# Performance work log

Measured on AMD Instinct MI355X. Metric: run time of the kernel, lower is better.

The kernel has to match this reference:

```python
import jax, jax.numpy as jnp
import numpy as np

D_MODEL = 1024
N_LAYERS = 4
D_INNER = 2 * D_MODEL          # expand=2
D_STATE = 16
D_CONV = 4
DT_RANK = D_MODEL // 16        # ceil(1024/16)=64
B, T = 2, 1024


def setup_inputs() -> dict:
    key = jax.random.key(0)
    ks = jax.random.split(key, 8)
    s = 0.02
    return {
        "x": jax.random.normal(ks[0], (B, T, D_MODEL), jnp.float32),
        "in_proj_w": jax.random.normal(ks[1], (N_LAYERS, 2 * D_INNER, D_MODEL), jnp.float32) * s,
        "conv_w": jax.random.normal(ks[2], (N_LAYERS, D_INNER, D_CONV), jnp.float32) * s,
        "conv_b": jnp.zeros((N_LAYERS, D_INNER), jnp.float32),
        "x_proj_w": jax.random.normal(ks[3], (N_LAYERS, DT_RANK + 2 * D_STATE, D_INNER), jnp.float32) * s,
        "dt_proj_w": jax.random.normal(ks[4], (N_LAYERS, D_INNER, DT_RANK), jnp.float32) * s,
        "dt_proj_b": jax.random.normal(ks[5], (N_LAYERS, D_INNER), jnp.float32) * 0.1,
        "A_log": jnp.tile(jnp.log(jnp.arange(1.0, D_STATE + 1.0, dtype=jnp.float32)), (N_LAYERS, D_INNER, 1)),
        "Dd": jnp.ones((N_LAYERS, D_INNER), jnp.float32),
        "out_proj_w": jax.random.normal(ks[6], (N_LAYERS, D_MODEL, D_INNER), jnp.float32) * s,
        "norm_w": jnp.ones((D_MODEL,), jnp.float32),
        "norm_b": jnp.zeros((D_MODEL,), jnp.float32),
    }


def _silu(v):
    return v * jax.nn.sigmoid(v)


def _mamba_block(x, in_w, cw, cb, xp_w, dtp_w, dtp_b, A_log, Dv, out_w):
    # x: [B,T,d_model]
    xz = jnp.einsum('btd,ed->bte', x, in_w)            # [B,T,2*d_inner]
    u, z = jnp.split(xz, 2, axis=-1)                   # each [B,T,d_inner]
    # causal depthwise conv over time
    uc = jax.lax.conv_general_dilated(
        u.transpose(0, 2, 1),                          # [B,d_inner,T]
        cw[:, None, :],                                # [d_inner,1,K]
        window_strides=(1,), padding=[(D_CONV - 1, 0)],
        feature_group_count=D_INNER,
        dimension_numbers=('NCH', 'OIH', 'NCH'))
    uc = _silu(uc.transpose(0, 2, 1) + cb)             # [B,T,d_inner]
    x_dbl = jnp.einsum('btd,ed->bte', uc, xp_w)        # [B,T,dt_rank+2*d_state]
    dt_r = x_dbl[..., :DT_RANK]
    Bm = x_dbl[..., DT_RANK:DT_RANK + D_STATE]         # [B,T,d_state]
    Cm = x_dbl[..., DT_RANK + D_STATE:]                # [B,T,d_state]
    dt = jax.nn.softplus(jnp.einsum('btr,dr->btd', dt_r, dtp_w) + dtp_b)  # [B,T,d_inner]
    A = -jnp.exp(A_log)                                # [d_inner,d_state]

    def step(h, inp):
        u_t, dt_t, B_t, C_t = inp                      # [B,dI],[B,dI],[B,dS],[B,dS]
        h = jnp.exp(dt_t[..., None] * A) * h + (dt_t * u_t)[..., None] * B_t[:, None, :]
        return h, jnp.einsum('bds,bs->bd', h, C_t)

    h0 = jnp.zeros((x.shape[0], D_INNER, D_STATE), x.dtype)
    xs = (uc.transpose(1, 0, 2), dt.transpose(1, 0, 2), Bm.transpose(1, 0, 2), Cm.transpose(1, 0, 2))
    _, ys = jax.lax.scan(step, h0, xs)                 # ys: [T,B,d_inner]
    y = ys.transpose(1, 0, 2) + uc * Dv                # skip term D*u
    y = y * _silu(z)                                   # gated
    return jnp.einsum('btd,ed->bte', y, out_w)         # [B,T,d_model]


def reference(x, in_proj_w, conv_w, conv_b, x_proj_w, dt_proj_w, dt_proj_b, A_log, Dd, out_proj_w, norm_w, norm_b):
    for i in range(in_proj_w.shape[0]):
        residual = x
        x = _mamba_block(x, in_proj_w[i], conv_w[i], conv_b[i], x_proj_w[i],
                         dt_proj_w[i], dt_proj_b[i], A_log[i], Dd[i], out_proj_w[i])
        x = x + residual
    mu = jnp.mean(x, -1, keepdims=True)
    var = jnp.var(x, -1, keepdims=True)
    return (x - mu) / jnp.sqrt(var + 1e-5) * norm_w + norm_b
```

## Files before the change

### kernel.cpp

```cpp
#include <hip/hip_runtime.h>
#include <hip/hip_bf16.h>

#define N_LAYERS 4
#define D_MODEL  1024
#define D_INNER  2048
#define D_STATE  16
#define D_CONV   4
#define DT_RANK  64
#define BB       2
#define TT       1024
#define BT       (BB*TT)

#define NCHUNK 32
#define SCTC   (TT/NCHUNK)
#define TB     8

#define XP_KS  8

typedef unsigned short ushort_t;
typedef __attribute__((ext_vector_type(8))) short short8;
typedef __attribute__((ext_vector_type(8))) unsigned short ushort8_t;
typedef __attribute__((ext_vector_type(4))) float f32x4;

__device__ __forceinline__ float sigmoidf_(float x){ return 1.f/(1.f+__expf(-x)); }
__device__ __forceinline__ float siluf_(float x){ return x*sigmoidf_(x); }
__device__ __forceinline__ float softplusf_(float x){ return fmaxf(x,0.f) + log1pf(__expf(-fabsf(x))); }
__device__ __forceinline__ ushort_t f2b(float f){
    unsigned int x = __builtin_bit_cast(unsigned int, f);
    unsigned int r = (x + 0x7fffu + ((x>>16)&1u)) >> 16;
    return (ushort_t)r;
}
__device__ __forceinline__ float b2f(ushort_t u){
    unsigned int x = ((unsigned int)u) << 16;
    return __builtin_bit_cast(float, x);
}

#define GLOAD(g, l) __builtin_amdgcn_global_load_lds( \
    (const __attribute__((address_space(1))) void*)(g), \
    (__attribute__((address_space(3))) void*)(l), 16, 0, 0)

__global__ __launch_bounds__(256) void f2ball_k(
    const float* __restrict__ x, const float* __restrict__ in_w,
    const float* __restrict__ out_w, const float* __restrict__ dtp_w,
    ushort_t* __restrict__ xinb, ushort_t* __restrict__ winb,
    ushort_t* __restrict__ woutb, ushort_t* __restrict__ dtpb)
{
    const int n0 = (BT*1024)/8;
    const int n1 = (N_LAYERS*4096*1024)/8;
    const int n2 = (N_LAYERS*1024*2048)/8;
    int i = blockIdx.x*256 + threadIdx.x;
    const float4* src; ushort8_t* dst; int j;
    if (i < n0){ src=(const float4*)x; dst=(ushort8_t*)xinb; j=i; }
    else if (i < n0+n1){ src=(const float4*)in_w; dst=(ushort8_t*)winb; j=i-n0; }
    else if (i < n0+n1+n2){ src=(const float4*)out_w; dst=(ushort8_t*)woutb; j=i-n0-n1; }
    else { src=(const float4*)dtp_w; dst=(ushort8_t*)dtpb; j=i-n0-n1-n2; }
    float4 v0 = src[2*j], v1 = src[2*j+1];
    ushort8_t o;
    o[0]=f2b(v0.x); o[1]=f2b(v0.y); o[2]=f2b(v0.z); o[3]=f2b(v0.w);
    o[4]=f2b(v1.x); o[5]=f2b(v1.y); o[6]=f2b(v1.z); o[7]=f2b(v1.w);
    dst[j] = o;
}

__global__ __launch_bounds__(512) void gemm_ip(
    const ushort_t* __restrict__ A, const ushort_t* __restrict__ W,
    int M, int N, int K, ushort_t* __restrict__ outb,
    int RM, int RN, int XN)
{
    __shared__ ushort_t As[4][128*32];
    __shared__ ushort_t Ws[4][128*32];
    const int tid  = threadIdx.x;
    const int lane = tid & 63;
    const int wv   = tid >> 6;
    const int wm0  = (wv>>2)*64, wn0 = (wv&3)*32;

    const int bid = blockIdx.x;
    const int xcd = bid & 7, bi = bid >> 3;
    const int xm = xcd / XN, xn = xcd - xm*XN;
    const int m0 = (xm*RM + bi/RN)*128;
    const int n0 = (xn*RN + bi - (bi/RN)*RN)*128;

    const int r0 = tid>>2, ch = tid&3;

    f32x4 acc[4][2];
    #pragma unroll
    for (int i=0;i<4;++i)
        #pragma unroll
        for (int j=0;j<2;++j) acc[i][j] = (f32x4){0.f,0.f,0.f,0.f};

    const int row_a = lane & 15, kc = (lane>>4)*8;
    const ushort_t* gA = A + (size_t)(m0+r0)*K + ch*8;
    const ushort_t* gW = W + (size_t)(n0+r0)*K + ch*8;

#define STAGE(KT, BUF) { \
    GLOAD(gA + (KT)*32, (char*)&As[BUF][0] + tid*16); \
    GLOAD(gW + (KT)*32, (char*)&Ws[BUF][0] + tid*16); }

#define COMPUTE(BUF) { \
    short8 af[4], bf[2]; \
    _Pragma("unroll") \
    for (int i=0;i<4;++i) af[i] = *(const short8*)&As[BUF][(wm0 + i*16 + row_a)*32 + kc]; \
    _Pragma("unroll") \
    for (int j=0;j<2;++j) bf[j] = *(const short8*)&Ws[BUF][(wn0 + j*16 + row_a)*32 + kc]; \
    __builtin_amdgcn_s_setprio(1); \
    _Pragma("unroll") \
    for (int i=0;i<4;++i) \
        _Pragma("unroll") \
        for (int j=0;j<2;++j) \
            acc[i][j] = __builtin_amdgcn_mfma_f32_16x16x32_bf16(af[i], bf[j], acc[i][j], 0,0,0); \
    __builtin_amdgcn_s_setprio(0); }

    const int nt = K >> 5;
    STAGE(0, 0); STAGE(1, 1); STAGE(2, 2);
    for (int t = 0; t < nt-3; ++t){
        asm volatile("s_waitcnt vmcnt(4)" ::: "memory");
        asm volatile("s_barrier" ::: "memory");
        STAGE(t+3, (t+3)&3);
        COMPUTE(t&3);
    }
    asm volatile("s_waitcnt vmcnt(4)" ::: "memory");
    asm volatile("s_barrier" ::: "memory");
    COMPUTE((nt-3)&3);
    asm volatile("s_waitcnt vmcnt(2)" ::: "memory");
    asm volatile("s_barrier" ::: "memory");
    COMPUTE((nt-2)&3);
    asm volatile("s_waitcnt vmcnt(0)" ::: "memory");
    asm volatile("s_barrier" ::: "memory");
    COMPUTE((nt-1)&3);
#undef STAGE
#undef COMPUTE

    const int crow = (lane>>4)*4, ccol = lane & 15;
    #pragma unroll
    for (int i=0;i<4;++i){
        #pragma unroll
        for (int j=0;j<2;++j){
            #pragma unroll
            for (int r=0;r<4;++r){
                int m = m0 + wm0 + i*16 + crow + r;
                int n = n0 + wn0 + j*16 + ccol;
                outb[(size_t)m*N + n] = f2b(acc[i][j][r]);
            }
        }
    }
}

__global__ __launch_bounds__(256) void gemm_op(
    const ushort_t* __restrict__ A, const ushort_t* __restrict__ W,
    float* __restrict__ C, int M, int N, int K,
    const float* __restrict__ res, ushort_t* __restrict__ outb,
    int RM, int RN, int XN)
{
    __shared__ ushort_t As[6][64*32];
    __shared__ ushort_t Ws[6][64*32];
    const int tid  = threadIdx.x;
    const int lane = tid & 63;
    const int wv   = tid >> 6;
    const int wm0  = (wv>>1)*32, wn0 = (wv&1)*32;

    const int bid = blockIdx.x;
    const int xcd = bid & 7, bi = bid >> 3;
    const int xm = xcd / XN, xn = xcd - xm*XN;
    const int m0 = (xm*RM + bi/RN)*64;
    const int n0 = (xn*RN + bi - (bi/RN)*RN)*64;

    const int r0 = tid>>2, ch = tid&3;

    f32x4 acc[2][2];
    #pragma unroll
    for (int i=0;i<2;++i)
        #pragma unroll
        for (int j=0;j<2;++j) acc[i][j] = (f32x4){0.f,0.f,0.f,0.f};

    const int row_a = lane & 15, kc = (lane>>4)*8;
    const ushort_t* gA = A + (size_t)(m0+r0)*K + ch*8;
    const ushort_t* gW = W + (size_t)(n0+r0)*K + ch*8;

#define STAGE(KT, BUF) { \
    GLOAD(gA + (KT)*32, (char*)&As[BUF][0] + tid*16); \
    GLOAD(gW + (KT)*32, (char*)&Ws[BUF][0] + tid*16); }

#define COMPUTE(BUF) { \
    short8 af[2], bf[2]; \
    _Pragma("unroll") \
    for (int i=0;i<2;++i) af[i] = *(const short8*)&As[BUF][(wm0 + i*16 + row_a)*32 + kc]; \
    _Pragma("unroll") \
    for (int j=0;j<2;++j) bf[j] = *(const short8*)&Ws[BUF][(wn0 + j*16 + row_a)*32 + kc]; \
    _Pragma("unroll") \
    for (int i=0;i<2;++i) \
        _Pragma("unroll") \
        for (int j=0;j<2;++j) \
            acc[i][j] = __builtin_amdgcn_mfma_f32_16x16x32_bf16(af[i], bf[j], acc[i][j], 0,0,0); }

    const int np = K >> 6;
    STAGE(0, 0); STAGE(1, 1);
    STAGE(2, 2); STAGE(3, 3);
    for (int p = 0; p < np-2; ++p){
        const int bA = (p%3)*2, bS = ((p+2)%3)*2;
        asm volatile("s_waitcnt vmcnt(4)" ::: "memory");
        asm volatile("s_barrier" ::: "memory");
        STAGE(2*p+4, bS); STAGE(2*p+5, bS+1);
        __builtin_amdgcn_s_setprio(1);
        COMPUTE(bA); COMPUTE(bA+1);
        __builtin_amdgcn_s_setprio(0);
    }
    {
        const int bA = ((np-2)%3)*2;
        asm volatile("s_waitcnt vmcnt(4)" ::: "memory");
        asm volatile("s_barrier" ::: "memory");
        COMPUTE(bA); COMPUTE(bA+1);
    }
    {
        const int bA = ((np-1)%3)*2;
        asm volatile("s_waitcnt vmcnt(0)" ::: "memory");
        asm volatile("s_barrier" ::: "memory");
        COMPUTE(bA); COMPUTE(bA+1);
    }
#undef STAGE
#undef COMPUTE

    const int crow = (lane>>4)*4, ccol = lane & 15;
    #pragma unroll
    for (int i=0;i<2;++i){
        #pragma unroll
        for (int j=0;j<2;++j){
            #pragma unroll
            for (int r=0;r<4;++r){
                int m = m0 + wm0 + i*16 + crow + r;
                int n = n0 + wn0 + j*16 + ccol;
                float v = acc[i][j][r] + res[(size_t)m*N + n];
                C[(size_t)m*N + n] = v;
                outb[(size_t)m*N + n] = f2b(v);
            }
        }
    }
}

__global__ __launch_bounds__(256) void dt_mfma(
    const ushort_t* __restrict__ A, const ushort_t* __restrict__ W,
    const float* __restrict__ bias, ushort_t* __restrict__ dtb, int N)
{
    __shared__ ushort_t As[2][64*32];
    __shared__ ushort_t Ws[2][64*32];
    const int tid = threadIdx.x, lane = tid&63, wv = tid>>6;
    const int wm0 = (wv>>1)*32, wn0 = (wv&1)*32;
    const int m0 = blockIdx.y*64, n0 = blockIdx.x*64;
    const int r0 = tid>>2, ch = tid&3;
    const ushort_t* gA = A + (size_t)(m0+r0)*64 + ch*8;
    const ushort_t* gW = W + (size_t)(n0+r0)*64 + ch*8;
    GLOAD(gA,      (char*)&As[0][0] + tid*16);
    GLOAD(gW,      (char*)&Ws[0][0] + tid*16);
    GLOAD(gA + 32, (char*)&As[1][0] + tid*16);
    GLOAD(gW + 32, (char*)&Ws[1][0] + tid*16);

    f32x4 acc[2][2];
    #pragma unroll
    for (int i=0;i<2;++i)
        #pragma unroll
        for (int j=0;j<2;++j) acc[i][j] = (f32x4){0.f,0.f,0.f,0.f};

    asm volatile("s_waitcnt vmcnt(0)" ::: "memory");
    asm volatile("s_barrier" ::: "memory");
    const int row_a = lane&15, kc = (lane>>4)*8;
    #pragma unroll
    for (int buf=0; buf<2; ++buf){
        short8 af[2], bf[2];
        #pragma unroll
        for (int i=0;i<2;++i) af[i] = *(const short8*)&As[buf][(wm0 + i*16 + row_a)*32 + kc];
        #pragma unroll
        for (int j=0;j<2;++j) bf[j] = *(const short8*)&Ws[buf][(wn0 + j*16 + row_a)*32 + kc];
        #pragma unroll
        for (int i=0;i<2;++i)
            #pragma unroll
            for (int j=0;j<2;++j)
                acc[i][j] = __builtin_amdgcn_mfma_f32_16x16x32_bf16(af[i], bf[j], acc[i][j], 0,0,0);
    }

    const int crow = (lane>>4)*4, ccol = lane & 15;
    #pragma unroll
    for (int i=0;i<2;++i){
        #pragma unroll
        for (int j=0;j<2;++j){
            #pragma unroll
            for (int r=0;r<4;++r){
                int m = m0 + wm0 + i*16 + crow + r;
                int n = n0 + wn0 + j*16 + ccol;
                float v = softplusf_(acc[i][j][r] + bias[n]);
                dtb[(size_t)m*N + n] = f2b(v);
            }
        }
    }
}

__global__ __launch_bounds__(256) void conv_silu_k(
    const ushort_t* __restrict__ xzb, const float* __restrict__ cw,
    const float* __restrict__ cb, ushort_t* __restrict__ ucb)
{
    int idx = blockIdx.x*256 + threadIdx.x;
    int d8 = (idx & 255) << 3;
    int bt = idx >> 8;
    int t  = bt & (TT-1);
    ushort8_t z8 = (ushort8_t)0;
    ushort8_t r0 = (t>=3) ? *(const ushort8_t*)(xzb + (size_t)(bt-3)*4096 + d8) : z8;
    ushort8_t r1 = (t>=2) ? *(const ushort8_t*)(xzb + (size_t)(bt-2)*4096 + d8) : z8;
    ushort8_t r2 = (t>=1) ? *(const ushort8_t*)(xzb + (size_t)(bt-1)*4096 + d8) : z8;
    ushort8_t r3 = *(const ushort8_t*)(xzb + (size_t)bt*4096 + d8);
    ushort8_t o;
    #pragma unroll
    for (int j=0;j<8;++j){
        float4 w4 = *(const float4*)(cw + (size_t)(d8+j)*4);
        float a = cb[d8+j];
        a = fmaf(b2f(r0[j]), w4.x, a);
        a = fmaf(b2f(r1[j]), w4.y, a);
        a = fmaf(b2f(r2[j]), w4.z, a);
        a = fmaf(b2f(r3[j]), w4.w, a);
        o[j] = f2b(siluf_(a));
    }
    *(ushort8_t*)(ucb + (size_t)bt*D_INNER + d8) = o;
}

__global__ __launch_bounds__(256) void gemm_tn_sk(
    const ushort_t* __restrict__ A, int lda,
    const float* __restrict__ W, int ldw,
    float* __restrict__ P, int M, int N, int K)
{
    __shared__ float As[16][68];
    __shared__ float Ws[16][68];
    const int tid = threadIdx.x;
    const int tx = tid & 15, ty = tid >> 4;
    const int m0 = blockIdx.y * 64, n0 = blockIdx.x * 64;
    const int kbase = blockIdx.z * (K/XP_KS);
    const int lr = tid >> 2;
    const int lk = (tid & 3) << 2;
    float acc[4][4] = {{0.f}};

    for (int kk = 0; kk < K/XP_KS; kk += 16) {
        int k0 = kbase + kk;
        ushort4 av4 = *(const ushort4*)(A + (size_t)(m0+lr)*lda + k0 + lk);
        float4 wv = make_float4(0.f,0.f,0.f,0.f);
        if (n0 + lr < N) wv = *(const float4*)(W + (size_t)(n0+lr)*ldw + k0 + lk);
        __syncthreads();
        As[lk+0][lr]=b2f(av4.x); As[lk+1][lr]=b2f(av4.y);
        As[lk+2][lr]=b2f(av4.z); As[lk+3][lr]=b2f(av4.w);
        Ws[lk+0][lr]=wv.x; Ws[lk+1][lr]=wv.y; Ws[lk+2][lr]=wv.z; Ws[lk+3][lr]=wv.w;
        __syncthreads();
        #pragma unroll
        for (int k = 0; k < 16; ++k) {
            float4 a = *(const float4*)&As[k][ty<<2];
            float4 b = *(const float4*)&Ws[k][tx<<2];
            float a4[4] = {a.x,a.y,a.z,a.w};
            float b4[4] = {b.x,b.y,b.z,b.w};
            #pragma unroll
            for (int i=0;i<4;++i)
                #pragma unroll
                for (int j=0;j<4;++j)
                    acc[i][j] = fmaf(a4[i], b4[j], acc[i][j]);
        }
    }

    float* Pz = P + (size_t)blockIdx.z * M * 96;
    #pragma unroll
    for (int i=0;i<4;++i){
        int m = m0 + (ty<<2) + i;
        #pragma unroll
        for (int j=0;j<4;++j){
            int n = n0 + (tx<<2) + j;
            if (n < N) Pz[(size_t)m*96 + n] = acc[i][j];
        }
    }
}

__global__ __launch_bounds__(256) void sk_reduce(
    const float* __restrict__ P, float* __restrict__ outp,
    ushort_t* __restrict__ dtrb, int MN)
{
    int g = blockIdx.x*256 + threadIdx.x;
    float s = 0.f;
    #pragma unroll
    for (int ks=0; ks<XP_KS; ++ks) s += P[(size_t)ks*MN + g];
    outp[g] = s;
    int m = g / 96, c = g - m*96;
    if (c < 64) dtrb[(size_t)m*64 + c] = f2b(s);
}


__global__ __launch_bounds__(256) void scan_p1(
    const ushort_t* __restrict__ dt, const ushort_t* __restrict__ uc,
    const float* __restrict__ xdbl, const float* __restrict__ A_log,
    float* __restrict__ hpart, float* __restrict__ hdecay)
{
    const int tid = threadIdx.x;
    const int d = blockIdx.x*256 + tid;
    const int b = blockIdx.y;
    const int k = blockIdx.z;
    const int t0 = k*SCTC;
    float A[16];
    #pragma unroll
    for (int q=0;q<4;++q){
        float4 v = *(const float4*)(A_log + (size_t)d*16 + q*4);
        A[q*4+0]=-__expf(v.x); A[q*4+1]=-__expf(v.y);
        A[q*4+2]=-__expf(v.z); A[q*4+3]=-__expf(v.w);
    }
    float h[16];
    #pragma unroll
    for (int s=0;s<16;++s) h[s]=0.f;
    float sumdt = 0.f;
    const ushort_t* dtp = dt + ((size_t)b*TT + t0)*D_INNER + d;
    const ushort_t* ucp = uc + ((size_t)b*TT + t0)*D_INNER + d;
    const float* bcp = xdbl + ((size_t)b*TT + t0)*96 + 64;
    #pragma unroll
    for (int tb=0; tb<SCTC; tb+=TB){
        float dtv[TB], ur[TB];
        #pragma unroll
        for (int j=0;j<TB;++j){
            dtv[j] = b2f(dtp[(size_t)(tb+j)*D_INNER]);
            ur[j]  = b2f(ucp[(size_t)(tb+j)*D_INNER]);
        }
        #pragma unroll
        for (int j=0;j<TB;++j){
            const float* bc = bcp + (size_t)(tb+j)*96;
            float du = dtv[j]*ur[j];
            sumdt += dtv[j];
            #pragma unroll
            for (int s=0;s<16;++s)
                h[s] = fmaf(__expf(dtv[j]*A[s]), h[s], du*bc[s]);
        }
    }
    size_t base = ((size_t)(k*BB+b)*D_INNER + d)*16;
    float4* hp = (float4*)(hpart + base);
    float4* hd = (float4*)(hdecay + base);
    #pragma unroll
    for (int q=0;q<4;++q){
        hp[q] = make_float4(h[q*4],h[q*4+1],h[q*4+2],h[q*4+3]);
        hd[q] = make_float4(__expf(sumdt*A[q*4+0]),__expf(sumdt*A[q*4+1]),
                            __expf(sumdt*A[q*4+2]),__expf(sumdt*A[q*4+3]));
    }
}

__global__ __launch_bounds__(256) void scan_fix(
    const float* __restrict__ hpart, const float* __restrict__ hdecay,
    float* __restrict__ hstart)
{
    int g = blockIdx.x*256 + threadIdx.x;
    float h = 0.f;
    #pragma unroll
    for (int k=0;k<NCHUNK;++k){
        size_t idx = (size_t)k*(BB*D_INNER*16) + g;
        hstart[idx] = h;
        h = fmaf(hdecay[idx], h, hpart[idx]);
    }
}

__global__ __launch_bounds__(256) void scan_p3(
    const ushort_t* __restrict__ dt, const ushort_t* __restrict__ uc,
    const float* __restrict__ xdbl, const float* __restrict__ A_log,
    const ushort_t* __restrict__ xzb, const float* __restrict__ Dd,
    const float* __restrict__ hstart, ushort_t* __restrict__ ysb)
{
    const int tid = threadIdx.x;
    const int d = blockIdx.x*256 + tid;
    const int b = blockIdx.y;
    const int k = blockIdx.z;
    const int t0 = k*SCTC;
    float A[16];
    #pragma unroll
    for (int q=0;q<4;++q){
        float4 v = *(const float4*)(A_log + (size_t)d*16 + q*4);
        A[q*4+0]=-__expf(v.x); A[q*4+1]=-__expf(v.y);
        A[q*4+2]=-__expf(v.z); A[q*4+3]=-__expf(v.w);
    }
    float h[16];
    {
        const float4* hs = (const float4*)(hstart + ((size_t)(k*BB+b)*D_INNER + d)*16);
        #pragma unroll
        for (int q=0;q<4;++q){
            float4 v = hs[q];
            h[q*4+0]=v.x; h[q*4+1]=v.y; h[q*4+2]=v.z; h[q*4+3]=v.w;
        }
    }
    const float Ddc = Dd[d];
    const ushort_t* dtp = dt + ((size_t)b*TT + t0)*D_INNER + d;
    const ushort_t* ucp = uc + ((size_t)b*TT + t0)*D_INNER + d;
    const ushort_t* zp  = xzb + ((size_t)b*TT + t0)*4096 + 2048 + d;
    const float* bcp = xdbl + ((size_t)b*TT + t0)*96 + 64;
    ushort_t* yp = ysb + ((size_t)b*TT + t0)*D_INNER + d;
    #pragma unroll
    for (int tb=0; tb<SCTC; tb+=TB){
        float dtv[TB], ur[TB], zr[TB];
        #pragma unroll
        for (int j=0;j<TB;++j){
            dtv[j] = b2f(dtp[(size_t)(tb+j)*D_INNER]);
            ur[j]  = b2f(ucp[(size_t)(tb+j)*D_INNER]);
            zr[j]  = b2f(zp [(size_t)(tb+j)*4096]);
        }
        #pragma unroll
        for (int j=0;j<TB;++j){
            const float* bc = bcp + (size_t)(tb+j)*96;
            float du = dtv[j]*ur[j];
            float y0=0.f,y1=0.f,y2=0.f,y3=0.f;
            #pragma unroll
            for (int q=0;q<4;++q){
                h[q*4+0] = fmaf(__expf(dtv[j]*A[q*4+0]), h[q*4+0], du*bc[q*4+0]);
                h[q*4+1] = fmaf(__expf(dtv[j]*A[q*4+1]), h[q*4+1], du*bc[q*4+1]);
                h[q*4+2] = fmaf(__expf(dtv[j]*A[q*4+2]), h[q*4+2], du*bc[q*4+2]);
                h[q*4+3] = fmaf(__expf(dtv[j]*A[q*4+3]), h[q*4+3], du*bc[q*4+3]);
            }
            #pragma unroll
            for (int q=0;q<4;++q){
                y0 = fmaf(h[q*4+0], bc[16+q*4+0], y0);
                y1 = fmaf(h[q*4+1], bc[16+q*4+1], y1);
                y2 = fmaf(h[q*4+2], bc[16+q*4+2], y2);
                y3 = fmaf(h[q*4+3], bc[16+q*4+3], y3);
            }
            float y = (y0+y1)+(y2+y3);
            float yv = (y + ur[j]*Ddc) * siluf_(zr[j]);
            yp[(size_t)(tb+j)*D_INNER] = f2b(yv);
        }
    }
}

__global__ __launch_bounds__(256) void layernorm_k(
    const float* __restrict__ X, const float* __restrict__ w,
    const float* __restrict__ b, float* __restrict__ out)
{
    int row = blockIdx.x;
    int tid = threadIdx.x;
    const float* xr = X + (size_t)row*D_MODEL;
    float4 v = *(const float4*)(xr + tid*4);
    float s  = v.x+v.y+v.z+v.w;
    float ss = fmaf(v.x,v.x, fmaf(v.y,v.y, fmaf(v.z,v.z, v.w*v.w)));
    #pragma unroll
    for (int off=32; off>0; off>>=1){
        s  += __shfl_down(s, off, 64);
        ss += __shfl_down(ss, off, 64);
    }
    __shared__ float red[8];
    int wid = tid>>6, lane = tid&63;
    if (lane==0){ red[wid]=s; red[4+wid]=ss; }
    __syncthreads();
    if (tid==0){
        float S  = red[0]+red[1]+red[2]+red[3];
        float SS = red[4]+red[5]+red[6]+red[7];
        float mu = S*(1.f/D_MODEL);
        float var = SS*(1.f/D_MODEL) - mu*mu;
        red[0]=mu; red[1]=rsqrtf(var + 1e-5f);
    }
    __syncthreads();
    float mu=red[0], rs=red[1];
    float4 wv = *(const float4*)(w + tid*4);
    float4 bv = *(const float4*)(b + tid*4);
    float4 o;
    o.x = fmaf((v.x-mu)*rs, wv.x, bv.x);
    o.y = fmaf((v.y-mu)*rs, wv.y, bv.y);
    o.z = fmaf((v.z-mu)*rs, wv.z, bv.z);
    o.w = fmaf((v.w-mu)*rs, wv.w, bv.w);
    *(float4*)(out + (size_t)row*D_MODEL + tid*4) = o;
}

extern "C" void kernel_launch(void* const* d_in, const int* in_sizes, int n_in,
                              void* d_out, int out_size, void* d_ws, size_t ws_size,
                              hipStream_t stream) {
    (void)in_sizes; (void)n_in; (void)out_size; (void)ws_size;
    const float* x      = (const float*)d_in[0];
    const float* in_w   = (const float*)d_in[1];
    const float* conv_w = (const float*)d_in[2];
    const float* conv_b = (const float*)d_in[3];
    const float* xp_w   = (const float*)d_in[4];
    const float* dtp_w  = (const float*)d_in[5];
    const float* dtp_b  = (const float*)d_in[6];
    const float* A_log  = (const float*)d_in[7];
    const float* Dd     = (const float*)d_in[8];
    const float* out_w  = (const float*)d_in[9];
    const float* nw     = (const float*)d_in[10];
    const float* nb     = (const float*)d_in[11];
    float* out = (float*)d_out;

    char* p = (char*)d_ws;
    ushort_t* xzb  = (ushort_t*)p; p += (size_t)BT*4096*2;
    ushort_t* ucb  = (ushort_t*)p; p += (size_t)BT*2048*2;
    float* xdbl    = (float*)p;  p += (size_t)BT*96*4;
    ushort_t* dtrb = (ushort_t*)p; p += (size_t)BT*64*2;
    ushort_t* dtbb = (ushort_t*)p; p += (size_t)BT*2048*2;
    float* xcur    = (float*)p;  p += (size_t)BT*1024*4;
    ushort_t* xinb = (ushort_t*)p; p += (size_t)BT*1024*2;
    ushort_t* ysb  = (ushort_t*)p; p += (size_t)BT*2048*2;
    ushort_t* winb = (ushort_t*)p; p += (size_t)N_LAYERS*4096*1024*2;
    ushort_t* woutb= (ushort_t*)p; p += (size_t)N_LAYERS*1024*2048*2;
    ushort_t* dtpb = (ushort_t*)p; p += (size_t)N_LAYERS*2048*64*2;
    float* hpart   = (float*)p;  p += (size_t)NCHUNK*BB*D_INNER*16*4;
    float* hdecay  = (float*)p;  p += (size_t)NCHUNK*BB*D_INNER*16*4;
    float* hstart  = (float*)p;  p += (size_t)NCHUNK*BB*D_INNER*16*4;
    float* pbuf    = hpart;

    f2ball_k<<<(BT*1024 + N_LAYERS*(4096*1024 + 1024*2048 + 2048*64))/2048,
               256,0,stream>>>(x, in_w, out_w, dtp_w, xinb, winb, woutb, dtpb);

    for (int i = 0; i < N_LAYERS; ++i){
        const float* xin = (i==0) ? x : xcur;
        const float* cw = conv_w + (size_t)i*D_INNER*D_CONV;
        const float* cb = conv_b + (size_t)i*D_INNER;
        gemm_ip<<<512,512,0,stream>>>(
            xinb, winb + (size_t)i*4096*1024, BT, 4096, D_MODEL, xzb, 8, 8, 4);
        conv_silu_k<<<BT,256,0,stream>>>(xzb, cw, cb, ucb);
        gemm_tn_sk<<<dim3(2,32,XP_KS),256,0,stream>>>(
            ucb, D_INNER, xp_w + (size_t)i*96*D_INNER, D_INNER,
            pbuf, BT, 96, D_INNER);
        sk_reduce<<<(BT*96)/256,256,0,stream>>>(pbuf, xdbl, dtrb, BT*96);
        dt_mfma<<<dim3(D_INNER/64, BT/64),256,0,stream>>>(
            dtrb, dtpb + (size_t)i*2048*64, dtp_b + (size_t)i*D_INNER, dtbb, D_INNER);
        scan_p1<<<dim3(D_INNER/256, BB, NCHUNK),256,0,stream>>>(
            dtbb, ucb, xdbl, A_log + (size_t)i*D_INNER*D_STATE, hpart, hdecay);
        scan_fix<<<(BB*D_INNER*16)/256,256,0,stream>>>(hpart, hdecay, hstart);
        scan_p3<<<dim3(D_INNER/256, BB, NCHUNK),256,0,stream>>>(
            dtbb, ucb, xdbl, A_log + (size_t)i*D_INNER*D_STATE, xzb,
            Dd + (size_t)i*D_INNER, hstart, ysb);
        gemm_op<<<512,256,0,stream>>>(
            ysb, woutb + (size_t)i*1024*2048, xcur, BT, 1024, D_INNER,
            xin, xinb, 8, 8, 2);
    }
    layernorm_k<<<BT,256,0,stream>>>(xcur, nw, nb, out);
}
```

Before: 681.8 us.

## Fuse split-K reduce into dt projection and merge scan phases cooperatively

Folds the split-K partial-sum reduction of x_proj into the dt-projection MFMA kernel, so each block reduces its own A tile directly into shared memory in bf16. Column-0 blocks also write the B/C part of xdbl. The three scan kernels (chunk pass, carry fix, output pass) become one cooperative kernel separated by grid-wide syncs, removing several launches per layer. The trade-offs are that the partial sums are re-reduced by every column block, which adds redundant reads, and that grid syncs plus the cooperative launch add their own overhead. The cooperative launch also needs all 512 blocks to be co-resident.

```diff
diff --git a/kernel.cpp b/kernel.cpp
--- a/kernel.cpp
+++ b/kernel.cpp
@@ -1,5 +1,8 @@
 #include <hip/hip_runtime.h>
 #include <hip/hip_bf16.h>
+#include <hip/hip_cooperative_groups.h>
+
+namespace cg = cooperative_groups;
 
 #define N_LAYERS 4
 #define D_MODEL  1024
@@ -235,62 +238,6 @@
     }
 }
 
-__global__ __launch_bounds__(256) void dt_mfma(
-    const ushort_t* __restrict__ A, const ushort_t* __restrict__ W,
-    const float* __restrict__ bias, ushort_t* __restrict__ dtb, int N)
-{
-    __shared__ ushort_t As[2][64*32];
-    __shared__ ushort_t Ws[2][64*32];
-    const int tid = threadIdx.x, lane = tid&63, wv = tid>>6;
-    const int wm0 = (wv>>1)*32, wn0 = (wv&1)*32;
-    const int m0 = blockIdx.y*64, n0 = blockIdx.x*64;
-    const int r0 = tid>>2, ch = tid&3;
-    const ushort_t* gA = A + (size_t)(m0+r0)*64 + ch*8;
-    const ushort_t* gW = W + (size_t)(n0+r0)*64 + ch*8;
-    GLOAD(gA,      (char*)&As[0][0] + tid*16);
-    GLOAD(gW,      (char*)&Ws[0][0] + tid*16);
-    GLOAD(gA + 32, (char*)&As[1][0] + tid*16);
-    GLOAD(gW + 32, (char*)&Ws[1][0] + tid*16);
-
-    f32x4 acc[2][2];
-    #pragma unroll
-    for (int i=0;i<2;++i)
-        #pragma unroll
-        for (int j=0;j<2;++j) acc[i][j] = (f32x4){0.f,0.f,0.f,0.f};
-
-    asm volatile("s_waitcnt vmcnt(0)" ::: "memory");
-    asm volatile("s_barrier" ::: "memory");
-    const int row_a = lane&15, kc = (lane>>4)*8;
-    #pragma unroll
-    for (int buf=0; buf<2; ++buf){
-        short8 af[2], bf[2];
-        #pragma unroll
-        for (int i=0;i<2;++i) af[i] = *(const short8*)&As[buf][(wm0 + i*16 + row_a)*32 + kc];
-        #pragma unroll
-        for (int j=0;j<2;++j) bf[j] = *(const short8*)&Ws[buf][(wn0 + j*16 + row_a)*32 + kc];
-        #pragma unroll
-        for (int i=0;i<2;++i)
-            #pragma unroll
-            for (int j=0;j<2;++j)
-                acc[i][j] = __builtin_amdgcn_mfma_f32_16x16x32_bf16(af[i], bf[j], acc[i][j], 0,0,0);
-    }
-
-    const int crow = (lane>>4)*4, ccol = lane & 15;
-    #pragma unroll
-    for (int i=0;i<2;++i){
-        #pragma unroll
-        for (int j=0;j<2;++j){
-            #pragma unroll
-            for (int r=0;r<4;++r){
-                int m = m0 + wm0 + i*16 + crow + r;
-                int n = n0 + wn0 + j*16 + ccol;
-                float v = softplusf_(acc[i][j][r] + bias[n]);
-                dtb[(size_t)m*N + n] = f2b(v);
-            }
-        }
-    }
-}
-
 __global__ __launch_bounds__(256) void conv_silu_k(
     const ushort_t* __restrict__ xzb, const float* __restrict__ cw,
     const float* __restrict__ cb, ushort_t* __restrict__ ucb)
@@ -369,25 +316,107 @@
     }
 }
 
-__global__ __launch_bounds__(256) void sk_reduce(
-    const float* __restrict__ P, float* __restrict__ outp,
-    ushort_t* __restrict__ dtrb, int MN)
-{
-    int g = blockIdx.x*256 + threadIdx.x;
-    float s = 0.f;
-    #pragma unroll
-    for (int ks=0; ks<XP_KS; ++ks) s += P[(size_t)ks*MN + g];
-    outp[g] = s;
-    int m = g / 96, c = g - m*96;
-    if (c < 64) dtrb[(size_t)m*64 + c] = f2b(s);
-}
-
-
-__global__ __launch_bounds__(256) void scan_p1(
+__global__ __launch_bounds__(256) void skred_dt(
+    const float* __restrict__ P,
+    const ushort_t* __restrict__ Wb,
+    const float* __restrict__ bias,
+    float* __restrict__ xdbl,
+    ushort_t* __restrict__ dtb)
+{
+    __shared__ ushort_t As[2][64*32];
+    __shared__ ushort_t Ws[2][64*32];
+    const int tid = threadIdx.x, lane = tid&63, wv = tid>>6;
+    const int wm0 = (wv>>1)*32, wn0 = (wv&1)*32;
+    const int n0 = blockIdx.x*64, m0 = blockIdx.y*64;
+    const int r0 = tid>>2, ch = tid&3;
+
+    const ushort_t* gW = Wb + (size_t)(n0+r0)*64 + ch*8;
+    GLOAD(gW,      (char*)&Ws[0][0] + tid*16);
+    GLOAD(gW + 32, (char*)&Ws[1][0] + tid*16);
+
+    const int ar = tid>>2, ac0 = (tid&3)*16;
+    float s[16];
+    #pragma unroll
+    for (int j=0;j<16;++j) s[j]=0.f;
+    const float* Pb = P + (size_t)(m0+ar)*96 + ac0;
+    #pragma unroll
+    for (int ks=0; ks<XP_KS; ++ks){
+        const float4* q = (const float4*)(Pb + (size_t)ks*BT*96);
+        float4 v0=q[0], v1=q[1], v2=q[2], v3=q[3];
+        s[0]+=v0.x; s[1]+=v0.y; s[2]+=v0.z; s[3]+=v0.w;
+        s[4]+=v1.x; s[5]+=v1.y; s[6]+=v1.z; s[7]+=v1.w;
+        s[8]+=v2.x; s[9]+=v2.y; s[10]+=v2.z; s[11]+=v2.w;
+        s[12]+=v3.x; s[13]+=v3.y; s[14]+=v3.z; s[15]+=v3.w;
+    }
+    ushort8_t o0, o1;
+    #pragma unroll
+    for (int j=0;j<8;++j){ o0[j]=f2b(s[j]); o1[j]=f2b(s[8+j]); }
+    const int abuf = ac0>>5, acc_ = ac0&31;
+    *(ushort8_t*)&As[abuf][ar*32 + acc_]     = o0;
+    *(ushort8_t*)&As[abuf][ar*32 + acc_ + 8] = o1;
+
+    if (blockIdx.x == 0){
+        const int rr = tid>>2, c2 = (tid&3)*8;
+        const float* Pc = P + (size_t)(m0+rr)*96 + 64 + c2;
+        float4 a0 = make_float4(0.f,0.f,0.f,0.f);
+        float4 a1 = make_float4(0.f,0.f,0.f,0.f);
+        #pragma unroll
+        for (int ks=0; ks<XP_KS; ++ks){
+            const float4* q = (const float4*)(Pc + (size_t)ks*BT*96);
+            float4 v0=q[0], v1=q[1];
+            a0.x+=v0.x; a0.y+=v0.y; a0.z+=v0.z; a0.w+=v0.w;
+            a1.x+=v1.x; a1.y+=v1.y; a1.z+=v1.z; a1.w+=v1.w;
+        }
+        *(float4*)(xdbl + (size_t)(m0+rr)*96 + 64 + c2)     = a0;
+        *(float4*)(xdbl + (size_t)(m0+rr)*96 + 64 + c2 + 4) = a1;
+    }
+
+    __syncthreads();
+
+    f32x4 acc[2][2];
+    #pragma unroll
+    for (int i=0;i<2;++i)
+        #pragma unroll
+        for (int j=0;j<2;++j) acc[i][j] = (f32x4){0.f,0.f,0.f,0.f};
+    const int row_a = lane&15, kc = (lane>>4)*8;
+    #pragma unroll
+    for (int buf=0; buf<2; ++buf){
+        short8 af[2], bf[2];
+        #pragma unroll
+        for (int i=0;i<2;++i) af[i] = *(const short8*)&As[buf][(wm0 + i*16 + row_a)*32 + kc];
+        #pragma unroll
+        for (int j=0;j<2;++j) bf[j] = *(const short8*)&Ws[buf][(wn0 + j*16 + row_a)*32 + kc];
+        #pragma unroll
+        for (int i=0;i<2;++i)
+            #pragma unroll
+            for (int j=0;j<2;++j)
+                acc[i][j] = __builtin_amdgcn_mfma_f32_16x16x32_bf16(af[i], bf[j], acc[i][j], 0,0,0);
+    }
+
+    const int crow = (lane>>4)*4, ccol = lane & 15;
+    #pragma unroll
+    for (int i=0;i<2;++i){
+        #pragma unroll
+        for (int j=0;j<2;++j){
+            #pragma unroll
+            for (int r=0;r<4;++r){
+                int m = m0 + wm0 + i*16 + crow + r;
+                int n = n0 + wn0 + j*16 + ccol;
+                float v = softplusf_(acc[i][j][r] + bias[n]);
+                dtb[(size_t)m*D_INNER + n] = f2b(v);
+            }
+        }
+    }
+}
+
+__global__ __launch_bounds__(256) void scan_all(
     const ushort_t* __restrict__ dt, const ushort_t* __restrict__ uc,
     const float* __restrict__ xdbl, const float* __restrict__ A_log,
-    float* __restrict__ hpart, float* __restrict__ hdecay)
-{
+    const ushort_t* __restrict__ xzb, const float* __restrict__ Dd,
+    float* __restrict__ hpart, float* __restrict__ hdecay,
+    float* __restrict__ hstart, ushort_t* __restrict__ ysb)
+{
+    cg::grid_group gg = cg::this_grid();
     const int tid = threadIdx.x;
     const int d = blockIdx.x*256 + tid;
     const int b = blockIdx.y;
@@ -400,120 +429,102 @@
         A[q*4+0]=-__expf(v.x); A[q*4+1]=-__expf(v.y);
         A[q*4+2]=-__expf(v.z); A[q*4+3]=-__expf(v.w);
     }
-    float h[16];
-    #pragma unroll
-    for (int s=0;s<16;++s) h[s]=0.f;
-    float sumdt = 0.f;
     const ushort_t* dtp = dt + ((size_t)b*TT + t0)*D_INNER + d;
     const ushort_t* ucp = uc + ((size_t)b*TT + t0)*D_INNER + d;
     const float* bcp = xdbl + ((size_t)b*TT + t0)*96 + 64;
-    #pragma unroll
-    for (int tb=0; tb<SCTC; tb+=TB){
-        float dtv[TB], ur[TB];
-        #pragma unroll
-        for (int j=0;j<TB;++j){
-            dtv[j] = b2f(dtp[(size_t)(tb+j)*D_INNER]);
-            ur[j]  = b2f(ucp[(size_t)(tb+j)*D_INNER]);
-        }
-        #pragma unroll
-        for (int j=0;j<TB;++j){
-            const float* bc = bcp + (size_t)(tb+j)*96;
-            float du = dtv[j]*ur[j];
-            sumdt += dtv[j];
-            #pragma unroll
-            for (int s=0;s<16;++s)
-                h[s] = fmaf(__expf(dtv[j]*A[s]), h[s], du*bc[s]);
-        }
-    }
-    size_t base = ((size_t)(k*BB+b)*D_INNER + d)*16;
-    float4* hp = (float4*)(hpart + base);
-    float4* hd = (float4*)(hdecay + base);
-    #pragma unroll
-    for (int q=0;q<4;++q){
-        hp[q] = make_float4(h[q*4],h[q*4+1],h[q*4+2],h[q*4+3]);
-        hd[q] = make_float4(__expf(sumdt*A[q*4+0]),__expf(sumdt*A[q*4+1]),
-                            __expf(sumdt*A[q*4+2]),__expf(sumdt*A[q*4+3]));
-    }
-}
-
-__global__ __launch_bounds__(256) void scan_fix(
-    const float* __restrict__ hpart, const float* __restrict__ hdecay,
-    float* __restrict__ hstart)
-{
-    int g = blockIdx.x*256 + threadIdx.x;
-    float h = 0.f;
-    #pragma unroll
-    for (int k=0;k<NCHUNK;++k){
-        size_t idx = (size_t)k*(BB*D_INNER*16) + g;
-        hstart[idx] = h;
-        h = fmaf(hdecay[idx], h, hpart[idx]);
-    }
-}
-
-__global__ __launch_bounds__(256) void scan_p3(
-    const ushort_t* __restrict__ dt, const ushort_t* __restrict__ uc,
-    const float* __restrict__ xdbl, const float* __restrict__ A_log,
-    const ushort_t* __restrict__ xzb, const float* __restrict__ Dd,
-    const float* __restrict__ hstart, ushort_t* __restrict__ ysb)
-{
-    const int tid = threadIdx.x;
-    const int d = blockIdx.x*256 + tid;
-    const int b = blockIdx.y;
-    const int k = blockIdx.z;
-    const int t0 = k*SCTC;
-    float A[16];
-    #pragma unroll
-    for (int q=0;q<4;++q){
-        float4 v = *(const float4*)(A_log + (size_t)d*16 + q*4);
-        A[q*4+0]=-__expf(v.x); A[q*4+1]=-__expf(v.y);
-        A[q*4+2]=-__expf(v.z); A[q*4+3]=-__expf(v.w);
-    }
-    float h[16];
+    const size_t hbase = ((size_t)(k*BB+b)*D_INNER + d)*16;
+
     {
-        const float4* hs = (const float4*)(hstart + ((size_t)(k*BB+b)*D_INNER + d)*16);
+        float h[16];
+        #pragma unroll
+        for (int s=0;s<16;++s) h[s]=0.f;
+        float sumdt = 0.f;
+        #pragma unroll
+        for (int tb=0; tb<SCTC; tb+=TB){
+            float dtv[TB], ur[TB];
+            #pragma unroll
+            for (int j=0;j<TB;++j){
+                dtv[j] = b2f(dtp[(size_t)(tb+j)*D_INNER]);
+                ur[j]  = b2f(ucp[(size_t)(tb+j)*D_INNER]);
+            }
+            #pragma unroll
+            for (int j=0;j<TB;++j){
+                const float* bc = bcp + (size_t)(tb+j)*96;
+                float du = dtv[j]*ur[j];
+                sumdt += dtv[j];
+                #pragma unroll
+                for (int s=0;s<16;++s)
+                    h[s] = fmaf(__expf(dtv[j]*A[s]), h[s], du*bc[s]);
+            }
+        }
+        float4* hp = (float4*)(hpart + hbase);
+        float4* hd = (float4*)(hdecay + hbase);
+        #pragma unroll
+        for (int q=0;q<4;++q){
+            hp[q] = make_float4(h[q*4],h[q*4+1],h[q*4+2],h[q*4+3]);
+            hd[q] = make_float4(__expf(sumdt*A[q*4+0]),__expf(sumdt*A[q*4+1]),
+                                __expf(sumdt*A[q*4+2]),__expf(sumdt*A[q*4+3]));
+        }
+    }
+    gg.sync();
+
+    {
+        int gl = ((blockIdx.z*BB + blockIdx.y)*8 + blockIdx.x)*256 + tid;
+        if (gl < BB*D_INNER*16){
+            float hh = 0.f;
+            #pragma unroll
+            for (int kk=0; kk<NCHUNK; ++kk){
+                size_t idx = (size_t)kk*(BB*D_INNER*16) + gl;
+                hstart[idx] = hh;
+                hh = fmaf(hdecay[idx], hh, hpart[idx]);
+            }
+        }
+    }
+    gg.sync();
+
+    {
+        float h[16];
+        const float4* hs = (const float4*)(hstart + hbase);
         #pragma unroll
         for (int q=0;q<4;++q){
             float4 v = hs[q];
             h[q*4+0]=v.x; h[q*4+1]=v.y; h[q*4+2]=v.z; h[q*4+3]=v.w;
         }
-    }
-    const float Ddc = Dd[d];
-    const ushort_t* dtp = dt + ((size_t)b*TT + t0)*D_INNER + d;
-    const ushort_t* ucp = uc + ((size_t)b*TT + t0)*D_INNER + d;
-    const ushort_t* zp  = xzb + ((size_t)b*TT + t0)*4096 + 2048 + d;
-    const float* bcp = xdbl + ((size_t)b*TT + t0)*96 + 64;
-    ushort_t* yp = ysb + ((size_t)b*TT + t0)*D_INNER + d;
-    #pragma unroll
-    for (int tb=0; tb<SCTC; tb+=TB){
-        float dtv[TB], ur[TB], zr[TB];
-        #pragma unroll
-        for (int j=0;j<TB;++j){
-            dtv[j] = b2f(dtp[(size_t)(tb+j)*D_INNER]);
-            ur[j]  = b2f(ucp[(size_t)(tb+j)*D_INNER]);
-            zr[j]  = b2f(zp [(size_t)(tb+j)*4096]);
-        }
-        #pragma unroll
-        for (int j=0;j<TB;++j){
-            const float* bc = bcp + (size_t)(tb+j)*96;
-            float du = dtv[j]*ur[j];
-            float y0=0.f,y1=0.f,y2=0.f,y3=0.f;
-            #pragma unroll
-            for (int q=0;q<4;++q){
-                h[q*4+0] = fmaf(__expf(dtv[j]*A[q*4+0]), h[q*4+0], du*bc[q*4+0]);
-                h[q*4+1] = fmaf(__expf(dtv[j]*A[q*4+1]), h[q*4+1], du*bc[q*4+1]);
-                h[q*4+2] = fmaf(__expf(dtv[j]*A[q*4+2]), h[q*4+2], du*bc[q*4+2]);
-                h[q*4+3] = fmaf(__expf(dtv[j]*A[q*4+3]), h[q*4+3], du*bc[q*4+3]);
-            }
-            #pragma unroll
-            for (int q=0;q<4;++q){
-                y0 = fmaf(h[q*4+0], bc[16+q*4+0], y0);
-                y1 = fmaf(h[q*4+1], bc[16+q*4+1], y1);
-                y2 = fmaf(h[q*4+2], bc[16+q*4+2], y2);
-                y3 = fmaf(h[q*4+3], bc[16+q*4+3], y3);
-            }
-            float y = (y0+y1)+(y2+y3);
-            float yv = (y + ur[j]*Ddc) * siluf_(zr[j]);
-            yp[(size_t)(tb+j)*D_INNER] = f2b(yv);
+        const float Ddc = Dd[d];
+        const ushort_t* zp = xzb + ((size_t)b*TT + t0)*4096 + 2048 + d;
+        ushort_t* yp = ysb + ((size_t)b*TT + t0)*D_INNER + d;
+        #pragma unroll
+        for (int tb=0; tb<SCTC; tb+=TB){
+            float dtv[TB], ur[TB], zr[TB];
+            #pragma unroll
+            for (int j=0;j<TB;++j){
+                dtv[j] = b2f(dtp[(size_t)(tb+j)*D_INNER]);
+                ur[j]  = b2f(ucp[(size_t)(tb+j)*D_INNER]);
+                zr[j]  = b2f(zp [(size_t)(tb+j)*4096]);
+            }
+            #pragma unroll
+            for (int j=0;j<TB;++j){
+                const float* bc = bcp + (size_t)(tb+j)*96;
+                float du = dtv[j]*ur[j];
+                float y0=0.f,y1=0.f,y2=0.f,y3=0.f;
+                #pragma unroll
+                for (int q=0;q<4;++q){
+                    h[q*4+0] = fmaf(__expf(dtv[j]*A[q*4+0]), h[q*4+0], du*bc[q*4+0]);
+                    h[q*4+1] = fmaf(__expf(dtv[j]*A[q*4+1]), h[q*4+1], du*bc[q*4+1]);
+                    h[q*4+2] = fmaf(__expf(dtv[j]*A[q*4+2]), h[q*4+2], du*bc[q*4+2]);
+                    h[q*4+3] = fmaf(__expf(dtv[j]*A[q*4+3]), h[q*4+3], du*bc[q*4+3]);
+                }
+                #pragma unroll
+                for (int q=0;q<4;++q){
+                    y0 = fmaf(h[q*4+0], bc[16+q*4+0], y0);
+                    y1 = fmaf(h[q*4+1], bc[16+q*4+1], y1);
+                    y2 = fmaf(h[q*4+2], bc[16+q*4+2], y2);
+                    y3 = fmaf(h[q*4+3], bc[16+q*4+3], y3);
+                }
+                float y = (y0+y1)+(y2+y3);
+                float yv = (y + ur[j]*Ddc) * siluf_(zr[j]);
+                yp[(size_t)(tb+j)*D_INNER] = f2b(yv);
+            }
         }
     }
 }
@@ -578,7 +589,6 @@
     ushort_t* xzb  = (ushort_t*)p; p += (size_t)BT*4096*2;
     ushort_t* ucb  = (ushort_t*)p; p += (size_t)BT*2048*2;
     float* xdbl    = (float*)p;  p += (size_t)BT*96*4;
-    ushort_t* dtrb = (ushort_t*)p; p += (size_t)BT*64*2;
     ushort_t* dtbb = (ushort_t*)p; p += (size_t)BT*2048*2;
     float* xcur    = (float*)p;  p += (size_t)BT*1024*4;
     ushort_t* xinb = (ushort_t*)p; p += (size_t)BT*1024*2;
@@ -604,15 +614,22 @@
         gemm_tn_sk<<<dim3(2,32,XP_KS),256,0,stream>>>(
             ucb, D_INNER, xp_w + (size_t)i*96*D_INNER, D_INNER,
             pbuf, BT, 96, D_INNER);
-        sk_reduce<<<(BT*96)/256,256,0,stream>>>(pbuf, xdbl, dtrb, BT*96);
-        dt_mfma<<<dim3(D_INNER/64, BT/64),256,0,stream>>>(
-            dtrb, dtpb + (size_t)i*2048*64, dtp_b + (size_t)i*D_INNER, dtbb, D_INNER);
-        scan_p1<<<dim3(D_INNER/256, BB, NCHUNK),256,0,stream>>>(
-            dtbb, ucb, xdbl, A_log + (size_t)i*D_INNER*D_STATE, hpart, hdecay);
-        scan_fix<<<(BB*D_INNER*16)/256,256,0,stream>>>(hpart, hdecay, hstart);
-        scan_p3<<<dim3(D_INNER/256, BB, NCHUNK),256,0,stream>>>(
-            dtbb, ucb, xdbl, A_log + (size_t)i*D_INNER*D_STATE, xzb,
-            Dd + (size_t)i*D_INNER, hstart, ysb);
+        skred_dt<<<dim3(D_INNER/64, BT/64),256,0,stream>>>(
+            pbuf, dtpb + (size_t)i*2048*64, dtp_b + (size_t)i*D_INNER,
+            xdbl, dtbb);
+        {
+            const ushort_t* dt_a = dtbb;  const ushort_t* uc_a = ucb;
+            const float* xd_a = xdbl;
+            const float* al_a = A_log + (size_t)i*D_INNER*D_STATE;
+            const ushort_t* xz_a = xzb;
+            const float* dd_a = Dd + (size_t)i*D_INNER;
+            float* hp_a = hpart; float* hd_a = hdecay; float* hs_a = hstart;
+            ushort_t* ys_a = ysb;
+            void* kargs[] = {&dt_a, &uc_a, &xd_a, &al_a, &xz_a, &dd_a,
+                             &hp_a, &hd_a, &hs_a, &ys_a};
+            hipLaunchCooperativeKernel((const void*)scan_all,
+                dim3(D_INNER/256, BB, NCHUNK), dim3(256,1,1), kargs, 0, stream);
+        }
         gemm_op<<<512,256,0,stream>>>(
             ysb, woutb + (size_t)i*1024*2048, xcur, BT, 1024, D_INNER,
             xin, xinb, 8, 8, 2);
```

Result: slower. 1.238 ms (+81.5%).
